# Kernel optimization log

Measured on AMD Instinct MI355X. Metric: run time of the kernel, lower is better.

The kernel has to match this reference:

```python
import math
import jax, jax.numpy as jnp
import numpy as np

N_SENSORS = 4760
K = 16
HID = 64
D_LAT = 1024
D_PROJ = 128
POS_DIM = 96
FACE_DIM = 32
OUT_CH = 1
N_HEADS = 4
HEAD_DIM = D_PROJ // N_HEADS
N_TOKENS = 6
NUM_BANDS = POS_DIM // 6
B = 16


def _sinusoidal_pos_encoding(positions, num_bands):
    # positions: (N,3) numpy -> (N, num_bands*2*3)
    freq = (2.0 ** np.arange(num_bands, dtype=np.float32))
    encs = []
    for d in range(3):
        scaled = positions[:, d:d + 1] * freq[None, :] * (math.pi / 100.0)
        encs.append(np.sin(scaled))
        encs.append(np.cos(scaled))
    return np.concatenate(encs, axis=-1).astype(np.float32)


def setup_inputs() -> dict:
    rng = np.random.default_rng(0)
    positions = rng.uniform(-100.0, 100.0, (N_SENSORS, 3)).astype(np.float32)
    # kNN graph by 3D euclidean distance
    d2 = ((positions[:, None, :] - positions[None, :, :]) ** 2).sum(-1)
    knn = np.argsort(d2, axis=1)[:, :K].astype(np.int32)
    face_ids = rng.integers(0, 6, N_SENSORS).astype(np.int32)
    pos_embed = _sinusoidal_pos_encoding(positions, NUM_BANDS)  # (N,96)

    key = jax.random.key(0)
    ks = jax.random.split(key, 20)
    def lin(k, din, dout):
        k1, k2 = jax.random.split(k)
        lim = 1.0 / math.sqrt(din)
        W = jax.random.uniform(k1, (din, dout), jnp.float32, -lim, lim)
        b = jax.random.uniform(k2, (dout,), jnp.float32, -lim, lim)
        return W, b

    W_nbr, b_nbr = lin(ks[0], 2 + POS_DIM + FACE_DIM, HID)
    W_ql, b_ql = lin(ks[1], POS_DIM + FACE_DIM, HID)
    W_lat, b_lat = lin(ks[2], D_LAT, D_PROJ)
    W_lf, b_lf = lin(ks[3], FACE_DIM, D_PROJ)
    W_qg, b_qg = lin(ks[4], POS_DIM + FACE_DIM, D_PROJ)
    W_k, b_k = lin(ks[5], D_PROJ, D_PROJ)
    W_v, b_v = lin(ks[6], D_PROJ, D_PROJ)
    W_go, b_go = lin(ks[7], D_PROJ, D_PROJ)
    W_m1, b_m1 = lin(ks[8], HID + D_PROJ, HID)
    W_m2, b_m2 = lin(ks[9], HID, OUT_CH)
    face_emb = jax.random.normal(ks[10], (6, FACE_DIM), jnp.float32)
    ln_g = jnp.ones((HID + D_PROJ,), jnp.float32)
    ln_b = jnp.zeros((HID + D_PROJ,), jnp.float32)

    x_flat = jax.random.normal(ks[11], (B, N_SENSORS, 2), jnp.float32)
    latent_seq = jax.random.normal(ks[12], (B, N_TOKENS, D_LAT), jnp.float32)
    mask = jax.random.randint(ks[13], (B, N_SENSORS), 0, 2, jnp.int32)

    return dict(x_flat=x_flat, latent_seq=latent_seq, pos_embed=jnp.asarray(pos_embed),
                face_emb=face_emb, W_nbr=W_nbr, b_nbr=b_nbr, W_ql=W_ql, b_ql=b_ql,
                W_lat=W_lat, b_lat=b_lat, W_lf=W_lf, b_lf=b_lf, W_qg=W_qg, b_qg=b_qg,
                W_k=W_k, b_k=b_k, W_v=W_v, b_v=b_v, W_go=W_go, b_go=b_go,
                ln_g=ln_g, ln_b=ln_b, W_m1=W_m1, b_m1=b_m1, W_m2=W_m2, b_m2=b_m2,
                mask=mask, knn_indices=jnp.asarray(knn), face_ids=jnp.asarray(face_ids))


def _forward(x_flat, latent_seq, pos_embed, face_emb,
             W_nbr, b_nbr, W_ql, b_ql, W_lat, b_lat, W_lf, b_lf,
             W_qg, b_qg, W_k, b_k, W_v, b_v, W_go, b_go,
             ln_g, ln_b, W_m1, b_m1, W_m2, b_m2,
             mask, knn_indices, face_ids):
    # Dense equivalent: compute prediction for every (b, n), zero out unmasked.
    # query: (N, pos+face)
    query = jnp.concatenate([pos_embed, face_emb[face_ids]], axis=-1)  # (N,128)

    # ---- local kNN attention ----
    nbr_values = x_flat[:, knn_indices, :]                 # (B,N,K,2)
    nbr_pos = pos_embed[knn_indices]                       # (N,K,96)
    nbr_face = face_emb[face_ids[knn_indices]]             # (N,K,32)
    nbr_static = jnp.broadcast_to(
        jnp.concatenate([nbr_pos, nbr_face], axis=-1)[None],
        (x_flat.shape[0], N_SENSORS, K, POS_DIM + FACE_DIM))
    nbr_feat = jnp.concatenate([nbr_values, nbr_static], axis=-1)  # (B,N,K,130)
    nbr_feat = nbr_feat @ W_nbr + b_nbr                    # (B,N,K,H)

    nbr_is_masked = mask[:, knn_indices] != 0              # (B,N,K) bool
    q_local = query @ W_ql + b_ql                          # (N,H)
    scale = HID ** (-0.5)
    logits = jnp.einsum('bnkh,nh->bnk', nbr_feat, q_local) * scale
    logits = jnp.where(nbr_is_masked, -10000.0, logits)
    attn = jax.nn.softmax(logits, axis=-1)
    local_feat = jnp.einsum('bnk,bnkh->bnh', attn, nbr_feat)  # (B,N,H)

    # ---- global cross-attention over 6 latent tokens ----
    latent_p = latent_seq @ W_lat + b_lat                  # (B,T,P)
    face_bias = face_emb[jnp.arange(N_TOKENS)] @ W_lf + b_lf  # (T,P)
    latent_kv = latent_p + face_bias[None]                 # (B,T,P)
    q_g = (query @ W_qg + b_qg).reshape(N_SENSORS, N_HEADS, HEAD_DIM)
    k_g = (latent_kv @ W_k + b_k).reshape(-1, N_TOKENS, N_HEADS, HEAD_DIM)
    v_g = (latent_kv @ W_v + b_v).reshape(-1, N_TOKENS, N_HEADS, HEAD_DIM)
    g_logits = jnp.einsum('nhd,bthd->bnht', q_g, k_g) * (HEAD_DIM ** (-0.5))
    g_attn = jax.nn.softmax(g_logits, axis=-1)
    g_feat = jnp.einsum('bnht,bthd->bnhd', g_attn, v_g)
    g_feat = g_feat.reshape(-1, N_SENSORS, D_PROJ) @ W_go + b_go  # (B,N,P)

    # ---- prediction MLP: LayerNorm -> Linear -> GELU -> Linear ----
    combined = jnp.concatenate([local_feat, g_feat], axis=-1)  # (B,N,H+P)
    mu = combined.mean(-1, keepdims=True)
    var = combined.var(-1, keepdims=True)
    normed = (combined - mu) * jax.lax.rsqrt(var + 1e-5) * ln_g + ln_b
    h = jax.nn.gelu(normed @ W_m1 + b_m1, approximate=False)
    preds = h @ W_m2 + b_m2                                # (B,N,out)

    return preds * (mask != 0)[..., None].astype(preds.dtype)


def reference(x_flat, latent_seq, pos_embed, face_emb,
              W_nbr, b_nbr, W_ql, b_ql, W_lat, b_lat, W_lf, b_lf,
              W_qg, b_qg, W_k, b_k, W_v, b_v, W_go, b_go,
              ln_g, ln_b, W_m1, b_m1, W_m2, b_m2,
              mask, knn_indices, face_ids):
    return _forward(x_flat, latent_seq, pos_embed, face_emb,
                    W_nbr, b_nbr, W_ql, b_ql, W_lat, b_lat, W_lf, b_lf,
                    W_qg, b_qg, W_k, b_k, W_v, b_v, W_go, b_go,
                    ln_g, ln_b, W_m1, b_m1, W_m2, b_m2,
                    mask, knn_indices, face_ids)
```

## Files before the change

kernel.cpp:

```cpp
#include <hip/hip_runtime.h>
#include <math.h>

#define NSN 4760
#define KNN 16
#define NT 6
#define NB 16
#define NGB 595
#define NBLK 85

__device__ __forceinline__ float rl_f(float v, int lane) {
  return __builtin_bit_cast(float, __builtin_amdgcn_readlane(__builtin_bit_cast(int, v), lane));
}

__global__ void precompute_all(const float* __restrict__ pos_emb,
    const float* __restrict__ face_emb, const int* __restrict__ face_ids,
    const float* __restrict__ W_nbr, const float* __restrict__ b_nbr,
    const float* __restrict__ W_ql, const float* __restrict__ b_ql,
    const float* __restrict__ W_qg, const float* __restrict__ b_qg,
    const float* __restrict__ latent,
    const float* __restrict__ W_lat, const float* __restrict__ b_lat,
    const float* __restrict__ W_lf, const float* __restrict__ b_lf,
    const float* __restrict__ W_k, const float* __restrict__ b_k,
    const float* __restrict__ W_v, const float* __restrict__ b_v,
    const float* __restrict__ W_go, const float* __restrict__ b_go,
    const float* __restrict__ W_m1, const float* __restrict__ b_m1,
    const float* __restrict__ ln_g, const float* __restrict__ ln_b,
    float* __restrict__ S, float* __restrict__ qlocal,
    float* __restrict__ qg, float* __restrict__ c01, float2* __restrict__ SS,
    float* __restrict__ kg, float4* __restrict__ TBL, float* __restrict__ C)
{
  __shared__ __align__(16) float qL[8][128];
  __shared__ __align__(16) float lat[1024];
  __shared__ __align__(16) float part[4][128];
  __shared__ __align__(16) float kvS[128];
  __shared__ __align__(16) float vrow[128];
  __shared__ __align__(16) float vwl[4][128];
  __shared__ __align__(16) float ghl[128];
  const int bid = blockIdx.x;
  const int tid = threadIdx.x;

  if (bid < 595) {
    const int w = tid >> 6, lane = tid & 63;
    const int n = bid * 8 + w;
    const int fid = face_ids[n];
    const int e1 = lane + 64;
    qL[w][lane] = pos_emb[n * 96 + lane];
    qL[w][e1] = (e1 < 96) ? pos_emb[n * 96 + e1] : face_emb[fid * 32 + (e1 - 96)];
    float s  = b_nbr[lane], ql = b_ql[lane];
    float g0 = b_qg[lane],  g1 = b_qg[lane + 64];
    #pragma unroll 2
    for (int i = 0; i < 128; ++i) {
      const float qi = qL[w][i];
      s  += qi * W_nbr[(2 + i) * 64 + lane];
      ql += qi * W_ql[i * 64 + lane];
      g0 += qi * W_qg[i * 128 + lane];
      g1 += qi * W_qg[i * 128 + 64 + lane];
    }
    S[n * 64 + lane] = s;
    qlocal[n * 64 + lane] = ql;
    qg[n * 128 + lane] = g0;
    qg[n * 128 + 64 + lane] = g1;
    float p0 = W_nbr[lane] * ql, p1 = W_nbr[64 + lane] * ql;
    #pragma unroll
    for (int o = 32; o; o >>= 1) { p0 += __shfl_xor(p0, o); p1 += __shfl_xor(p1, o); }
    if (lane == 0) { c01[2 * n] = p0; c01[2 * n + 1] = p1; }
    qL[w][lane] = s * ln_g[lane];
    float sm = 0.f;
    #pragma unroll 2
    for (int h = 0; h < 64; ++h) {
      sm += qL[w][h] * W_m1[h * 64 + lane];
    }
    SS[n * 64 + lane] = make_float2(s, sm);
  } else if (bid < 691) {
    const int bt = bid - 595;
    const int t = bt % NT;
    const int chunk = tid >> 7, o = tid & 127;
    for (int i = tid; i < 1024; i += 512) lat[i] = latent[bt * 1024 + i];
    if (tid < 128) ghl[tid] = ln_g[64 + tid];
    __syncthreads();
    {
      float acc = 0.f;
      const int i0 = chunk * 256;
      #pragma unroll 4
      for (int i = 0; i < 256; ++i)
        acc += lat[i0 + i] * W_lat[(i0 + i) * 128 + o];
      part[chunk][o] = acc;
    }
    __syncthreads();
    if (tid < 128) {
      float acc = part[0][o] + part[1][o] + part[2][o] + part[3][o]
                + b_lat[o] + b_lf[o];
      #pragma unroll
      for (int i = 0; i < 32; ++i) acc += face_emb[t * 32 + i] * W_lf[i * 128 + o];
      kvS[o] = acc;
    }
    __syncthreads();
    {
      const float* Wx = (chunk < 2) ? W_k : W_v;
      const int i0 = (chunk & 1) * 64;
      float acc = 0.f;
      #pragma unroll 4
      for (int i = 0; i < 64; ++i)
        acc += kvS[i0 + i] * Wx[(i0 + i) * 128 + o];
      part[chunk][o] = acc;
    }
    __syncthreads();
    if (tid < 128) {
      kg[bt * 128 + o] = part[0][o] + part[1][o] + b_k[o];
    } else if (tid < 256) {
      vrow[o] = part[2][o] + part[3][o] + b_v[o];
    }
    __syncthreads();
    {
      float a = 0.f;
      #pragma unroll 8
      for (int i = 0; i < 32; ++i)
        a += vrow[chunk * 32 + i] * W_go[(chunk * 32 + i) * 128 + o];
      vwl[chunk][o] = a;
    }
    __syncthreads();
    if (tid < 256) {
      const int h = tid >> 6, oo = tid & 63;
      float m = 0.f;
      #pragma unroll 4
      for (int i = 0; i < 128; ++i)
        m += vwl[h][i] * ghl[i] * W_m1[(64 + i) * 64 + oo];
      TBL[(bt * 4 + h) * 64 + oo] =
          make_float4(vwl[h][2 * oo], vwl[h][2 * oo + 1], m, 0.f);
    }
  } else {
    const int o = tid;
    if (o < 64) {
      float wa = 0.f, wb = 0.f;
      #pragma unroll 4
      for (int h = 0; h < 64; ++h) {
        const float gw = ln_g[h] * W_m1[h * 64 + o];
        wa += W_nbr[h] * gw;
        wb += W_nbr[64 + h] * gw;
      }
      C[o] = wa; C[64 + o] = wb;
      float g = 0.f, p = 0.f;
      #pragma unroll 4
      for (int d = 0; d < 192; ++d) {
        const float w1 = W_m1[d * 64 + o];
        g += ln_g[d] * w1;
        p += ln_b[d] * w1;
      }
      C[128 + o] = g; C[192 + o] = p + b_m1[o];
      float c1 = 0.f;
      #pragma unroll 4
      for (int i = 0; i < 128; ++i)
        c1 += b_go[i] * ln_g[64 + i] * W_m1[(64 + i) * 64 + o];
      C[256 + o] = c1;
    }
  }
}

__global__ void precompute_D(const int* __restrict__ knn,
    const float* __restrict__ S, const float* __restrict__ qlocal,
    float* __restrict__ D)
{
  const int idx = blockIdx.x * 256 + threadIdx.x;
  const int n = idx >> 4;
  if (n >= NSN) return;
  const int j = knn[idx];
  const float4* Sr = (const float4*)(S + j * 64);
  const float4* Qr = (const float4*)(qlocal + n * 64);
  float acc = 0.f;
  #pragma unroll 4
  for (int i = 0; i < 16; ++i) {
    const float4 a = Sr[i]; const float4 q = Qr[i];
    acc += a.x * q.x + a.y * q.y + a.z * q.z + a.w * q.w;
  }
  D[idx] = acc;
}

__launch_bounds__(256, 2)
__global__ void precompute_item(const int* __restrict__ knn,
    const float* __restrict__ D, const float* __restrict__ c01,
    const float* __restrict__ x_flat, const int* __restrict__ mask,
    const float* __restrict__ qg, const float* __restrict__ kg,
    float* __restrict__ ATT, float2* __restrict__ AX, float* __restrict__ GAW)
{
  const int i = blockIdx.x * 256 + threadIdx.x;
  if (i >= NB * NSN) return;
  const int b = i / NSN;
  const int n = i - b * NSN;

  int j[16];
  {
    const int4* kr = (const int4*)(knn + n * 16);
    const int4 a = kr[0], bb = kr[1], c = kr[2], d = kr[3];
    j[0]=a.x; j[1]=a.y; j[2]=a.z; j[3]=a.w;
    j[4]=bb.x; j[5]=bb.y; j[6]=bb.z; j[7]=bb.w;
    j[8]=c.x; j[9]=c.y; j[10]=c.z; j[11]=c.w;
    j[12]=d.x; j[13]=d.y; j[14]=d.z; j[15]=d.w;
  }
  float dg[16];
  {
    const float4* dr = (const float4*)(D + n * 16);
    const float4 a = dr[0], bb = dr[1], c = dr[2], d = dr[3];
    dg[0]=a.x; dg[1]=a.y; dg[2]=a.z; dg[3]=a.w;
    dg[4]=bb.x; dg[5]=bb.y; dg[6]=bb.z; dg[7]=bb.w;
    dg[8]=c.x; dg[9]=c.y; dg[10]=c.z; dg[11]=c.w;
    dg[12]=d.x; dg[13]=d.y; dg[14]=d.z; dg[15]=d.w;
  }
  const float2 cv = *(const float2*)(c01 + 2 * n);
  const float* xb = x_flat + (size_t)b * NSN * 2;
  const int* mb = mask + b * NSN;
  float x0[16], x1[16], lg[16];
  #pragma unroll 4
  for (int k = 0; k < 16; ++k) {
    const float2 xv = *(const float2*)(xb + 2 * j[k]);
    const int mk = mb[j[k]];
    x0[k] = xv.x; x1[k] = xv.y;
    const float l = (dg[k] + xv.x * cv.x + xv.y * cv.y) * 0.125f;
    lg[k] = (mk != 0) ? -10000.0f : l;
  }
  float mx = lg[0];
  #pragma unroll
  for (int k = 1; k < 16; ++k) mx = fmaxf(mx, lg[k]);
  float s = 0.f;
  #pragma unroll
  for (int k = 0; k < 16; ++k) { lg[k] = __expf(lg[k] - mx); s += lg[k]; }
  const float inv = 1.0f / s;
  float ax0 = 0.f, ax1 = 0.f;
  #pragma unroll
  for (int k = 0; k < 16; ++k) { lg[k] *= inv; ax0 += lg[k] * x0[k]; ax1 += lg[k] * x1[k]; }
  {
    float4* ao = (float4*)(ATT + (size_t)i * 16);
    ao[0] = make_float4(lg[0], lg[1], lg[2], lg[3]);
    ao[1] = make_float4(lg[4], lg[5], lg[6], lg[7]);
    ao[2] = make_float4(lg[8], lg[9], lg[10], lg[11]);
    ao[3] = make_float4(lg[12], lg[13], lg[14], lg[15]);
    AX[i] = make_float2(ax0, ax1);
  }

  const float* qgr = qg + n * 128;
  const float* kgb = kg + b * NT * 128;
  #pragma unroll 1
  for (int h = 0; h < 4; ++h) {
    float4 q[8];
    const float4* q4 = (const float4*)(qgr + h * 32);
    #pragma unroll
    for (int u = 0; u < 8; ++u) q[u] = q4[u];
    float p[NT];
    #pragma unroll
    for (int t = 0; t < NT; ++t) {
      const float4* k4 = (const float4*)(kgb + t * 128 + h * 32);
      float a = 0.f;
      #pragma unroll
      for (int u = 0; u < 8; ++u) {
        const float4 kv = k4[u];
        a += q[u].x * kv.x + q[u].y * kv.y + q[u].z * kv.z + q[u].w * kv.w;
      }
      p[t] = a * 0.17677669529663687f;
    }
    float m2 = p[0];
    #pragma unroll
    for (int t = 1; t < NT; ++t) m2 = fmaxf(m2, p[t]);
    float s2 = 0.f;
    #pragma unroll
    for (int t = 0; t < NT; ++t) { p[t] = __expf(p[t] - m2); s2 += p[t]; }
    const float i2 = 1.0f / s2;
    float* go = GAW + (size_t)i * 24 + h * 6;
    #pragma unroll
    for (int t = 0; t < NT; ++t) go[t] = p[t] * i2;
  }
}

__launch_bounds__(512, 4)
__global__ void fused_main(const int* __restrict__ mask,
    const int* __restrict__ knn, const float* __restrict__ Wnbr,
    const float2* __restrict__ SS, const float* __restrict__ ATT,
    const float2* __restrict__ AX, const float* __restrict__ GAW,
    const float4* __restrict__ TBL, const float* __restrict__ CONSTS,
    const float* __restrict__ bgo, const float* __restrict__ Wm2,
    const float* __restrict__ bm2, float* __restrict__ out)
{
  __shared__ __align__(16) float4 TBLl[NT * 4 * 64];

  const int tid = threadIdx.x;
  const int b = blockIdx.x / NBLK;
  const int bg = blockIdx.x - b * NBLK;
  {
    const float4* tb = TBL + b * (NT * 4 * 64);
    for (int i = tid; i < NT * 4 * 64; i += 512) TBLl[i] = tb[i];
  }
  __syncthreads();

  const int w = tid >> 6, lane = tid & 63;

  const float wa  = CONSTS[lane],       wbc = CONSTS[64 + lane];
  const float cg  = CONSTS[128 + lane], cp  = CONSTS[192 + lane];
  const float cc1 = CONSTS[256 + lane];
  const float w0 = Wnbr[lane], w1 = Wnbr[64 + lane];
  const float2 bgov = *(const float2*)(bgo + 2 * lane);
  const float wm2 = Wm2[lane], bm2s = bm2[0];

  #pragma unroll 1
  for (int ng = bg; ng < NGB; ng += NBLK) {
    const int n = ng * 8 + w;
    const int item = b * NSN + n;
    const int mself = mask[item];

    int jv = 0; float aw = 0.f;
    if (lane < 16) {
      jv = knn[n * 16 + lane];
      aw = ATT[(size_t)item * 16 + lane];
    }
    float gw = 0.f;
    if (lane < 24) gw = GAW[(size_t)item * 24 + lane];
    const float2 axv = AX[item];

    float lf = axv.x * w0 + axv.y * w1;
    float L  = axv.x * wa + axv.y * wbc;
    #pragma unroll
    for (int kb = 0; kb < 4; ++kb) {
      const int j0 = __builtin_amdgcn_readlane(jv, 4 * kb + 0);
      const int j1 = __builtin_amdgcn_readlane(jv, 4 * kb + 1);
      const int j2 = __builtin_amdgcn_readlane(jv, 4 * kb + 2);
      const int j3 = __builtin_amdgcn_readlane(jv, 4 * kb + 3);
      const float a0 = rl_f(aw, 4 * kb + 0);
      const float a1 = rl_f(aw, 4 * kb + 1);
      const float a2 = rl_f(aw, 4 * kb + 2);
      const float a3 = rl_f(aw, 4 * kb + 3);
      const float2 s0 = SS[j0 * 64 + lane];
      const float2 s1 = SS[j1 * 64 + lane];
      const float2 s2 = SS[j2 * 64 + lane];
      const float2 s3 = SS[j3 * 64 + lane];
      lf += a0 * s0.x + a1 * s1.x + a2 * s2.x + a3 * s3.x;
      L  += a0 * s0.y + a1 * s1.y + a2 * s2.y + a3 * s3.y;
    }

    float g0 = bgov.x, g1 = bgov.y, M = 0.f;
    #pragma unroll 2
    for (int t = 0; t < NT; ++t) {
      const float4 r0 = TBLl[(t * 4 + 0) * 64 + lane];
      const float4 r1 = TBLl[(t * 4 + 1) * 64 + lane];
      const float4 r2 = TBLl[(t * 4 + 2) * 64 + lane];
      const float4 r3 = TBLl[(t * 4 + 3) * 64 + lane];
      const float a0 = rl_f(gw, t);
      const float a1 = rl_f(gw, 6 + t);
      const float a2 = rl_f(gw, 12 + t);
      const float a3 = rl_f(gw, 18 + t);
      g0 += a0 * r0.x + a1 * r1.x + a2 * r2.x + a3 * r3.x;
      g1 += a0 * r0.y + a1 * r1.y + a2 * r2.y + a3 * r3.y;
      M  += a0 * r0.z + a1 * r1.z + a2 * r2.z + a3 * r3.z;
    }

    float s1 = lf + g0 + g1;
    float s2 = lf * lf + g0 * g0 + g1 * g1;
    #pragma unroll
    for (int o = 32; o; o >>= 1) { s1 += __shfl_xor(s1, o); s2 += __shfl_xor(s2, o); }
    const float mu  = s1 * (1.0f / 192.0f);
    const float var = s2 * (1.0f / 192.0f) - mu * mu;
    const float rinv = rsqrtf(var + 1e-5f);

    const float m1 = rinv * (L + M + cc1 - mu * cg) + cp;
    const float gelu = 0.5f * m1 * (1.0f + erff(m1 * 0.7071067811865476f));
    float pr = gelu * wm2;
    #pragma unroll
    for (int o = 32; o; o >>= 1) pr += __shfl_xor(pr, o);
    float res = pr + bm2s;
    if (mself == 0) res = 0.f;
    if (lane == 0) out[item] = res;
  }
}

extern "C" void kernel_launch(void* const* d_in, const int* in_sizes, int n_in,
                              void* d_out, int out_size, void* d_ws, size_t ws_size,
                              hipStream_t stream) {
  (void)in_sizes; (void)n_in; (void)out_size; (void)ws_size;
  const float* x_flat   = (const float*)d_in[0];
  const float* latent   = (const float*)d_in[1];
  const float* pos_emb  = (const float*)d_in[2];
  const float* face_emb = (const float*)d_in[3];
  const float* W_nbr = (const float*)d_in[4];
  const float* b_nbr = (const float*)d_in[5];
  const float* W_ql  = (const float*)d_in[6];
  const float* b_ql  = (const float*)d_in[7];
  const float* W_lat = (const float*)d_in[8];
  const float* b_lat = (const float*)d_in[9];
  const float* W_lf  = (const float*)d_in[10];
  const float* b_lf  = (const float*)d_in[11];
  const float* W_qg  = (const float*)d_in[12];
  const float* b_qg  = (const float*)d_in[13];
  const float* W_k   = (const float*)d_in[14];
  const float* b_k   = (const float*)d_in[15];
  const float* W_v   = (const float*)d_in[16];
  const float* b_v   = (const float*)d_in[17];
  const float* W_go  = (const float*)d_in[18];
  const float* b_go  = (const float*)d_in[19];
  const float* ln_g  = (const float*)d_in[20];
  const float* ln_b  = (const float*)d_in[21];
  const float* W_m1  = (const float*)d_in[22];
  const float* b_m1  = (const float*)d_in[23];
  const float* W_m2  = (const float*)d_in[24];
  const float* b_m2  = (const float*)d_in[25];
  const int* mask     = (const int*)d_in[26];
  const int* knn      = (const int*)d_in[27];
  const int* face_ids = (const int*)d_in[28];
  float* out = (float*)d_out;

  float* ws = (float*)d_ws;
  float* S      = ws;  ws += NSN * 64;
  float* qlocal = ws;  ws += NSN * 64;
  float* qgb    = ws;  ws += NSN * 128;
  float* c01    = ws;  ws += NSN * 2;
  float2* SSt   = (float2*)ws;  ws += NSN * 64 * 2;
  float* kgb    = ws;  ws += NB * NT * 128;
  float4* TBLt  = (float4*)ws;  ws += NB * NT * 4 * 64 * 4;
  float* CONSTS = ws;  ws += 5 * 64;
  float* Dt     = ws;  ws += NSN * KNN;
  float* ATTt   = ws;  ws += NB * NSN * KNN;
  float2* AXt   = (float2*)ws;  ws += NB * NSN * 2;
  float* GAWt   = ws;  ws += NB * NSN * 24;

  precompute_all<<<692, 512, 0, stream>>>(pos_emb, face_emb, face_ids,
      W_nbr, b_nbr, W_ql, b_ql, W_qg, b_qg,
      latent, W_lat, b_lat, W_lf, b_lf, W_k, b_k, W_v, b_v,
      W_go, b_go, W_m1, b_m1, ln_g, ln_b,
      S, qlocal, qgb, c01, SSt, kgb, TBLt, CONSTS);
  precompute_D<<<(NSN * KNN + 255) / 256, 256, 0, stream>>>(knn, S, qlocal, Dt);
  precompute_item<<<(NB * NSN + 255) / 256, 256, 0, stream>>>(knn, Dt, c01,
      x_flat, mask, qgb, kgb, ATTt, AXt, GAWt);
  fused_main<<<NB * NBLK, 512, 0, stream>>>(mask, knn, W_nbr,
      SSt, ATTt, AXt, GAWt, TBLt, CONSTS, b_go, W_m2, b_m2, out);
}
```

Before: 259.2 us.

## Reuse gathered neighbor SS rows across two batches per block in fused_main

Changes the fused_main work split: each block now handles one 8-sensor group for a pair of batches instead of looping over sensor groups within a single batch. The 16 neighbor SS rows are gathered once into registers and reused for both batch items, halving the random gather traffic. The cost is doubled shared table storage, more registers (launch bounds relaxed to 2 blocks/CU), and a larger grid of short-lived blocks whose table staging is amortized over only two items.

```diff
diff --git a/kernel.cpp b/kernel.cpp
--- a/kernel.cpp
+++ b/kernel.cpp
@@ -5,8 +5,6 @@
 #define KNN 16
 #define NT 6
 #define NB 16
-#define NGB 595
-#define NBLK 85
 
 __device__ __forceinline__ float rl_f(float v, int lane) {
   return __builtin_bit_cast(float, __builtin_amdgcn_readlane(__builtin_bit_cast(int, v), lane));
@@ -269,7 +267,7 @@
   }
 }
 
-__launch_bounds__(512, 4)
+__launch_bounds__(512, 2)
 __global__ void fused_main(const int* __restrict__ mask,
     const int* __restrict__ knn, const float* __restrict__ Wnbr,
     const float2* __restrict__ SS, const float* __restrict__ ATT,
@@ -278,18 +276,20 @@
     const float* __restrict__ bgo, const float* __restrict__ Wm2,
     const float* __restrict__ bm2, float* __restrict__ out)
 {
-  __shared__ __align__(16) float4 TBLl[NT * 4 * 64];
+  __shared__ __align__(16) float4 TBLl[2][NT * 4 * 64];
 
   const int tid = threadIdx.x;
-  const int b = blockIdx.x / NBLK;
-  const int bg = blockIdx.x - b * NBLK;
+  const int bp = blockIdx.x / 595;
+  const int ng = blockIdx.x - bp * 595;
+  const int b0 = bp * 2;
   {
-    const float4* tb = TBL + b * (NT * 4 * 64);
-    for (int i = tid; i < NT * 4 * 64; i += 512) TBLl[i] = tb[i];
+    const float4* tb = TBL + b0 * (NT * 4 * 64);
+    for (int i = tid; i < 2 * NT * 4 * 64; i += 512) TBLl[0][i] = tb[i];
   }
   __syncthreads();
 
   const int w = tid >> 6, lane = tid & 63;
+  const int n = ng * 8 + w;
 
   const float wa  = CONSTS[lane],       wbc = CONSTS[64 + lane];
   const float cg  = CONSTS[128 + lane], cp  = CONSTS[192 + lane];
@@ -298,17 +298,25 @@
   const float2 bgov = *(const float2*)(bgo + 2 * lane);
   const float wm2 = Wm2[lane], bm2s = bm2[0];
 
+  int jv = 0;
+  if (lane < 16) jv = knn[n * 16 + lane];
+  float2 ss[16];
+  #pragma unroll
+  for (int kb = 0; kb < 2; ++kb) {
+    int jj[8];
+    #pragma unroll
+    for (int q = 0; q < 8; ++q) jj[q] = __builtin_amdgcn_readlane(jv, kb * 8 + q);
+    #pragma unroll
+    for (int q = 0; q < 8; ++q) ss[kb * 8 + q] = SS[jj[q] * 64 + lane];
+  }
+
   #pragma unroll 1
-  for (int ng = bg; ng < NGB; ng += NBLK) {
-    const int n = ng * 8 + w;
-    const int item = b * NSN + n;
+  for (int bi = 0; bi < 2; ++bi) {
+    const int item = (b0 + bi) * NSN + n;
     const int mself = mask[item];
 
-    int jv = 0; float aw = 0.f;
-    if (lane < 16) {
-      jv = knn[n * 16 + lane];
-      aw = ATT[(size_t)item * 16 + lane];
-    }
+    float aw = 0.f;
+    if (lane < 16) aw = ATT[(size_t)item * 16 + lane];
     float gw = 0.f;
     if (lane < 24) gw = GAW[(size_t)item * 24 + lane];
     const float2 axv = AX[item];
@@ -316,30 +324,19 @@
     float lf = axv.x * w0 + axv.y * w1;
     float L  = axv.x * wa + axv.y * wbc;
     #pragma unroll
-    for (int kb = 0; kb < 4; ++kb) {
-      const int j0 = __builtin_amdgcn_readlane(jv, 4 * kb + 0);
-      const int j1 = __builtin_amdgcn_readlane(jv, 4 * kb + 1);
-      const int j2 = __builtin_amdgcn_readlane(jv, 4 * kb + 2);
-      const int j3 = __builtin_amdgcn_readlane(jv, 4 * kb + 3);
-      const float a0 = rl_f(aw, 4 * kb + 0);
-      const float a1 = rl_f(aw, 4 * kb + 1);
-      const float a2 = rl_f(aw, 4 * kb + 2);
-      const float a3 = rl_f(aw, 4 * kb + 3);
-      const float2 s0 = SS[j0 * 64 + lane];
-      const float2 s1 = SS[j1 * 64 + lane];
-      const float2 s2 = SS[j2 * 64 + lane];
-      const float2 s3 = SS[j3 * 64 + lane];
-      lf += a0 * s0.x + a1 * s1.x + a2 * s2.x + a3 * s3.x;
-      L  += a0 * s0.y + a1 * s1.y + a2 * s2.y + a3 * s3.y;
+    for (int k = 0; k < 16; ++k) {
+      const float a = rl_f(aw, k);
+      lf += a * ss[k].x;
+      L  += a * ss[k].y;
     }
 
     float g0 = bgov.x, g1 = bgov.y, M = 0.f;
     #pragma unroll 2
     for (int t = 0; t < NT; ++t) {
-      const float4 r0 = TBLl[(t * 4 + 0) * 64 + lane];
-      const float4 r1 = TBLl[(t * 4 + 1) * 64 + lane];
-      const float4 r2 = TBLl[(t * 4 + 2) * 64 + lane];
-      const float4 r3 = TBLl[(t * 4 + 3) * 64 + lane];
+      const float4 r0 = TBLl[bi][(t * 4 + 0) * 64 + lane];
+      const float4 r1 = TBLl[bi][(t * 4 + 1) * 64 + lane];
+      const float4 r2 = TBLl[bi][(t * 4 + 2) * 64 + lane];
+      const float4 r3 = TBLl[bi][(t * 4 + 3) * 64 + lane];
       const float a0 = rl_f(gw, t);
       const float a1 = rl_f(gw, 6 + t);
       const float a2 = rl_f(gw, 12 + t);
@@ -425,6 +422,6 @@
   precompute_D<<<(NSN * KNN + 255) / 256, 256, 0, stream>>>(knn, S, qlocal, Dt);
   precompute_item<<<(NB * NSN + 255) / 256, 256, 0, stream>>>(knn, Dt, c01,
       x_flat, mask, qgb, kgb, ATTt, AXt, GAWt);
-  fused_main<<<NB * NBLK, 512, 0, stream>>>(mask, knn, W_nbr,
+  fused_main<<<8 * 595, 512, 0, stream>>>(mask, knn, W_nbr,
       SSt, ATTt, AXt, GAWt, TBLt, CONSTS, b_go, W_m2, b_m2, out);
 }
```

Result: no change. 261.1 us (+0.7%).
